# Performance work log

Measured on AMD Instinct MI355X. Metric: run time of the kernel, lower is better.

Reference implementation:

```python
import jax, jax.numpy as jnp
import numpy as np

N_NODES = 100000
N_EDGES = 800000
N_FEAT = 64
H_DIM = 64
N_GRAPHS = 64


def _glorot(key, fan_in, fan_out):
    lim = np.sqrt(6.0 / (fan_in + fan_out)).astype(np.float32)
    return jax.random.uniform(key, (fan_in, fan_out), jnp.float32, -lim, lim)


def setup_inputs() -> dict:
    key = jax.random.key(0)
    ks = jax.random.split(key, 10)
    x = jax.random.normal(ks[0], (N_NODES, N_FEAT), jnp.float32)
    edge_index = jax.random.randint(ks[1], (2, N_EDGES), 0, N_NODES, dtype=jnp.int64)
    batch = jnp.sort(jax.random.randint(ks[2], (N_NODES,), 0, N_GRAPHS, dtype=jnp.int64))
    return {
        "x": x,
        "edge_index": edge_index,
        "batch": batch,
        "W0": _glorot(ks[3], N_FEAT, H_DIM), "b0": jnp.zeros((H_DIM,), jnp.float32),
        "W1": _glorot(ks[4], H_DIM, H_DIM), "b1": jnp.zeros((H_DIM,), jnp.float32),
        "W2": _glorot(ks[5], H_DIM, H_DIM), "b2": jnp.zeros((H_DIM,), jnp.float32),
        "Wl": _glorot(ks[6], H_DIM, H_DIM),
        "bl": jax.random.normal(ks[7], (H_DIM,), jnp.float32) * 0.01,
    }


def _gcn_conv(h, W, b, row, col, dinv_r, dinv_c, n_nodes):
    # PyG GCNConv: x W, then sym-normalized aggregation over edges+self-loops
    h = h @ W                                   # [N, H]
    msg = h[row] * (dinv_r * dinv_c)[:, None]   # gather + scale, [E+N, H]
    out = jax.ops.segment_sum(msg, col, num_segments=n_nodes)  # scatter-add
    return out + b


def reference(x, edge_index, batch, W0, b0, W1, b1, W2, b2, Wl, bl):
    n = x.shape[0]
    loops = jnp.arange(n, dtype=edge_index.dtype)
    row = jnp.concatenate([edge_index[0], loops])  # source nodes (+self-loops)
    col = jnp.concatenate([edge_index[1], loops])  # destination nodes
    deg = jax.ops.segment_sum(jnp.ones_like(col, dtype=x.dtype), col, num_segments=n)
    dinv = jnp.where(deg > 0, jax.lax.rsqrt(deg), 0.0)
    dinv_r, dinv_c = dinv[row], dinv[col]

    out = x
    for W, b in ((W0, b0), (W1, b1), (W2, b2)):
        out = jax.nn.relu(_gcn_conv(out, W, b, row, col, dinv_r, dinv_c, n))
        # F.dropout(training=False) is identity in eval mode
    return (out, out @ Wl + bl)
```

## Files before the change

### kernel.cpp

```cpp
#include <hip/hip_runtime.h>

#define NN 100000
#define NE 800000
#define HD 64
#define BK 128
#define NBUCK ((NN + BK - 1) / BK)
#define PA_EPT 16
#define PA_NB ((NE + 256 * PA_EPT - 1) / (256 * PA_EPT))
#define LDW 68
#define LDB 72

typedef __attribute__((ext_vector_type(8))) short bf16x8;
typedef __attribute__((ext_vector_type(4))) float f32x4;

__device__ __forceinline__ int load_idx(const void* ei, int i, bool is32) {
    if (is32) return ((const int*)ei)[i];
    return (int)(((const long long*)ei)[i]);
}

__device__ __forceinline__ unsigned short f2bf(float f) {
    unsigned u = __float_as_uint(f);
    return (unsigned short)((u + 0x7FFFu + ((u >> 16) & 1u)) >> 16);
}

__device__ __forceinline__ float bf2f(unsigned short h) {
    return __uint_as_float((unsigned)h << 16);
}

__device__ __forceinline__ void bfacc(const uint4& u, float4& a, float4& b) {
    a.x += __uint_as_float(u.x << 16);
    a.y += __uint_as_float(u.x & 0xFFFF0000u);
    a.z += __uint_as_float(u.y << 16);
    a.w += __uint_as_float(u.y & 0xFFFF0000u);
    b.x += __uint_as_float(u.z << 16);
    b.y += __uint_as_float(u.z & 0xFFFF0000u);
    b.z += __uint_as_float(u.w << 16);
    b.w += __uint_as_float(u.w & 0xFFFF0000u);
}

__global__ void k_initdet(const void* ei, int* bcnt, int* flag) {
    __shared__ int bad;
    int t = threadIdx.x;
    if (t == 0) bad = 0;
    if (t < NBUCK) bcnt[t] = 0;
    __syncthreads();
    const long long* p = (const long long*)ei;
    for (int i = t; i < 4096; i += 1024) {
        long long v = p[i];
        if (v < 0 || v >= (long long)NN) bad = 1;
    }
    __syncthreads();
    if (t == 0) *flag = bad ? 1 : 0;
}

__global__ __launch_bounds__(256) void k_pass0(const void* ei, const int* flag,
                                               int* bcnt) {
    __shared__ int h[NBUCK];
    for (int i = threadIdx.x; i < NBUCK; i += 256) h[i] = 0;
    __syncthreads();
    bool is32 = (*flag != 0);
    int stride = gridDim.x * 256;
    for (int e = blockIdx.x * 256 + threadIdx.x; e < NE; e += stride) {
        int dst = load_idx(ei, NE + e, is32);
        atomicAdd(&h[dst >> 7], 1);
    }
    __syncthreads();
    for (int i = threadIdx.x; i < NBUCK; i += 256) {
        int v = h[i];
        if (v) atomicAdd(&bcnt[i], v);
    }
}

__global__ __launch_bounds__(256) void k_scan1(const int* __restrict__ bcnt,
                                               int* __restrict__ offs,
                                               int* __restrict__ curs) {
    __shared__ int sc[256];
    int t = threadIdx.x;
    int v[4], s = 0;
#pragma unroll
    for (int i = 0; i < 4; ++i) {
        int b = t * 4 + i;
        v[i] = (b < NBUCK) ? bcnt[b] : 0;
        s += v[i];
    }
    sc[t] = s;
    __syncthreads();
    for (int off = 1; off < 256; off <<= 1) {
        int add = (t >= off) ? sc[t - off] : 0;
        __syncthreads();
        sc[t] += add;
        __syncthreads();
    }
    int run = sc[t] - s;
#pragma unroll
    for (int i = 0; i < 4; ++i) {
        int b = t * 4 + i;
        if (b < NBUCK) { offs[b] = run; curs[b] = run; }
        run += v[i];
    }
    if (t == 255) offs[NBUCK] = sc[255];
}

__global__ __launch_bounds__(256) void k_passA(const void* ei, const int* flag,
                                               int* curs, unsigned* ebuf) {
    __shared__ int h[NBUCK];
    __shared__ int base[NBUCK];
    for (int i = threadIdx.x; i < NBUCK; i += 256) h[i] = 0;
    __syncthreads();
    bool is32 = (*flag != 0);
    int e0 = blockIdx.x * (256 * PA_EPT);
    int src[PA_EPT], dst[PA_EPT];
#pragma unroll
    for (int i = 0; i < PA_EPT; ++i) {
        int e = e0 + i * 256 + threadIdx.x;
        if (e < NE) {
            src[i] = load_idx(ei, e, is32);
            dst[i] = load_idx(ei, NE + e, is32);
            atomicAdd(&h[dst[i] >> 7], 1);
        } else dst[i] = -1;
    }
    __syncthreads();
    for (int i = threadIdx.x; i < NBUCK; i += 256) {
        int v = h[i];
        base[i] = v ? atomicAdd(&curs[i], v) : 0;
        h[i] = 0;
    }
    __syncthreads();
#pragma unroll
    for (int i = 0; i < PA_EPT; ++i) {
        if (dst[i] >= 0) {
            int b = dst[i] >> 7;
            int p = base[b] + atomicAdd(&h[b], 1);
            ebuf[p] = (unsigned)src[i] | ((unsigned)(dst[i] & 127) << 17);
        }
    }
}

__global__ __launch_bounds__(256) void k_passB(const unsigned* __restrict__ ebuf,
                                               const int* __restrict__ offs,
                                               int* __restrict__ noffs,
                                               int* __restrict__ csr_src,
                                               float* __restrict__ dinv) {
    __shared__ int cnt[BK];
    __shared__ int sc[BK];
    __shared__ int nbase[BK];
    __shared__ int rank[BK];
    int bk = blockIdx.x;
    int t = threadIdx.x;
    if (t < BK) { cnt[t] = 0; rank[t] = 0; }
    __syncthreads();
    int rs = offs[bk], re = offs[bk + 1];
    for (int i = rs + t; i < re; i += 256)
        atomicAdd(&cnt[ebuf[i] >> 17], 1);
    __syncthreads();
    if (t < BK) sc[t] = cnt[t];
    __syncthreads();
    for (int off = 1; off < BK; off <<= 1) {
        int v = 0;
        if (t < BK && t >= off) v = sc[t - off];
        __syncthreads();
        if (t < BK) sc[t] += v;
        __syncthreads();
    }
    if (t < BK) {
        int node = bk * BK + t;
        int nb = rs + sc[t] - cnt[t];
        nbase[t] = nb;
        if (node < NN) {
            noffs[node] = nb;
            dinv[node] = rsqrtf((float)(cnt[t] + 1));
        }
    }
    if (bk == NBUCK - 1 && t == 0) noffs[NN] = re;
    __syncthreads();
    for (int i = rs + t; i < re; i += 256) {
        unsigned w = ebuf[i];
        int dl = w >> 17;
        int p = nbase[dl] + atomicAdd(&rank[dl], 1);
        csr_src[p] = (int)(w & 0x1FFFFu);
    }
}

template <bool BIAS, bool PRE, bool BF16OUT>
__global__ __launch_bounds__(256, 4) void k_gemm(const float* __restrict__ X,
                                                 const float* __restrict__ W,
                                                 const float* __restrict__ bias,
                                                 const float* __restrict__ dinv,
                                                 void* __restrict__ Hout, int n) {
    __shared__ float Ws[64 * LDW];
    __shared__ float Xs[128 * LDW];
    int t = threadIdx.x;
    int row0 = blockIdx.x * 128;
    const float4* X4 = (const float4*)X;
    for (int i = t; i < 64 * 16; i += 256) {
        float4 v = ((const float4*)W)[i];
        *(float4*)&Ws[(i >> 4) * LDW + (i & 15) * 4] = v;
    }
    for (int i = t; i < 128 * 16; i += 256) {
        int r = row0 + (i >> 4);
        float4 v = (r < n) ? X4[(size_t)r * 16 + (i & 15)]
                           : make_float4(0.f, 0.f, 0.f, 0.f);
        *(float4*)&Xs[(i >> 4) * LDW + (i & 15) * 4] = v;
    }
    __syncthreads();
    int tc = (t & 15) * 4;
    int rbase = t >> 4;
    float4 acc[8] = {};
#pragma unroll 1
    for (int k = 0; k < 64; k += 4) {
        float4 wv[4], xv[8];
#pragma unroll
        for (int kk = 0; kk < 4; ++kk)
            wv[kk] = *(const float4*)&Ws[(k + kk) * LDW + tc];
#pragma unroll
        for (int i = 0; i < 8; ++i)
            xv[i] = *(const float4*)&Xs[(rbase + 16 * i) * LDW + k];
#pragma unroll
        for (int i = 0; i < 8; ++i) {
            acc[i].x += xv[i].x * wv[0].x + xv[i].y * wv[1].x
                      + xv[i].z * wv[2].x + xv[i].w * wv[3].x;
            acc[i].y += xv[i].x * wv[0].y + xv[i].y * wv[1].y
                      + xv[i].z * wv[2].y + xv[i].w * wv[3].y;
            acc[i].z += xv[i].x * wv[0].z + xv[i].y * wv[1].z
                      + xv[i].z * wv[2].z + xv[i].w * wv[3].z;
            acc[i].w += xv[i].x * wv[0].w + xv[i].y * wv[1].w
                      + xv[i].z * wv[2].w + xv[i].w * wv[3].w;
        }
    }
    float4 bv = make_float4(0.f, 0.f, 0.f, 0.f);
    if (BIAS) bv = *(const float4*)&bias[tc];
#pragma unroll
    for (int i = 0; i < 8; ++i) {
        int r = row0 + rbase + 16 * i;
        if (r < n) {
            float s = PRE ? dinv[r] : 1.f;
            float4 o;
            o.x = (acc[i].x + bv.x) * s;
            o.y = (acc[i].y + bv.y) * s;
            o.z = (acc[i].z + bv.z) * s;
            o.w = (acc[i].w + bv.w) * s;
            if (BF16OUT) {
                ushort4 p;
                p.x = f2bf(o.x); p.y = f2bf(o.y); p.z = f2bf(o.z); p.w = f2bf(o.w);
                ((ushort4*)Hout)[(size_t)r * 16 + (t & 15)] = p;
            } else {
                ((float4*)Hout)[(size_t)r * 16 + (t & 15)] = o;
            }
        }
    }
}

template <int MODE>
__global__ __launch_bounds__(256, 5) void k_fused(const uint4* __restrict__ Hb,
                                               const int* __restrict__ noffs,
                                               const int* __restrict__ csr_src,
                                               const float* __restrict__ dinv,
                                               const float4* __restrict__ b4,
                                               const float* __restrict__ Wn,
                                               const float* __restrict__ bl,
                                               unsigned short* __restrict__ HbOut,
                                               float4* __restrict__ out0,
                                               float* __restrict__ out1) {
    __shared__ unsigned short WtH[64 * LDB];
    __shared__ unsigned short WtL[64 * LDB];
    __shared__ __align__(16) char scratch[32 * LDB * 2 * 2];
    __shared__ float dvs[32];
    __shared__ float bls[64];
    unsigned short* rows_hi = (unsigned short*)scratch;
    unsigned short* rows_lo = (unsigned short*)scratch + 32 * LDB;
    float* cbuf = (float*)scratch;
    int t = threadIdx.x;
    int lane = t & 63;
    int cl = lane >> 3;
    int q = lane & 7;
    int cbase = lane & ~7;
    int nl = (t >> 6) * 8 + cl;
    int base = blockIdx.x * 32;
    int node = base + nl;
    const char* hb8 = (const char*)Hb;
    unsigned qoff = (unsigned)(q << 4);

    float dv = 0.f;
    int e0 = 0, e1 = 0;
    uint4 uself = make_uint4(0u, 0u, 0u, 0u);
    if (node < NN) {
        dv = dinv[node];
        e0 = noffs[node];
        e1 = noffs[node + 1];
        uself = *(const uint4*)(hb8 + (((unsigned)node << 7) | qoff));
    }

    for (int i = t; i < 64 * 64; i += 256) {
        int k = i >> 6, c = i & 63;
        float wv = Wn[i];
        unsigned short hi = f2bf(wv);
        unsigned short lo = f2bf(wv - bf2f(hi));
        WtH[c * LDB + k] = hi;
        WtL[c * LDB + k] = lo;
    }
    if (MODE == 1 && t < 64) bls[t] = bl[t];

    float4 alo = make_float4(0.f, 0.f, 0.f, 0.f);
    float4 ahi = make_float4(0.f, 0.f, 0.f, 0.f);
    if (node < NN) {
        bfacc(uself, alo, ahi);
#pragma unroll 1
        for (int e = e0; e < e1; e += 8) {
            int rem = e1 - e;
            int idx = (q < rem) ? csr_src[e + q] : 0;
            unsigned off[8];
#pragma unroll
            for (int j = 0; j < 8; ++j)
                off[j] = ((unsigned)__shfl(idx, cbase + j, 64) << 7) | qoff;
            uint4 uu[8];
#pragma unroll
            for (int j = 0; j < 8; ++j)
                uu[j] = *(const uint4*)(hb8 + off[j]);
#pragma unroll
            for (int j = 0; j < 8; ++j)
                if (j < rem) bfacc(uu[j], alo, ahi);
        }
    }
    if (node < NN) {
        float4 b0v = b4[2 * q], b1v = b4[2 * q + 1];
        float f[8];
        f[0] = fmaxf(alo.x * dv + b0v.x, 0.f);
        f[1] = fmaxf(alo.y * dv + b0v.y, 0.f);
        f[2] = fmaxf(alo.z * dv + b0v.z, 0.f);
        f[3] = fmaxf(alo.w * dv + b0v.w, 0.f);
        f[4] = fmaxf(ahi.x * dv + b1v.x, 0.f);
        f[5] = fmaxf(ahi.y * dv + b1v.y, 0.f);
        f[6] = fmaxf(ahi.z * dv + b1v.z, 0.f);
        f[7] = fmaxf(ahi.w * dv + b1v.w, 0.f);
        if (MODE == 1) {
            out0[(size_t)node * 16 + 2 * q]     = make_float4(f[0], f[1], f[2], f[3]);
            out0[(size_t)node * 16 + 2 * q + 1] = make_float4(f[4], f[5], f[6], f[7]);
        }
        unsigned hw[4], lw[4];
#pragma unroll
        for (int i = 0; i < 4; ++i) {
            unsigned short h0 = f2bf(f[2 * i]),     h1 = f2bf(f[2 * i + 1]);
            unsigned short l0 = f2bf(f[2 * i]     - bf2f(h0));
            unsigned short l1 = f2bf(f[2 * i + 1] - bf2f(h1));
            hw[i] = (unsigned)h0 | ((unsigned)h1 << 16);
            lw[i] = (unsigned)l0 | ((unsigned)l1 << 16);
        }
        *(uint4*)&rows_hi[nl * LDB + 8 * q] = make_uint4(hw[0], hw[1], hw[2], hw[3]);
        *(uint4*)&rows_lo[nl * LDB + 8 * q] = make_uint4(lw[0], lw[1], lw[2], lw[3]);
        if (q == 0) dvs[nl] = dv;
    }
    __syncthreads();

    int w = t >> 6;
    int la = lane & 15, kc = lane >> 4;
    int tr = w & 1;
    int c0 = (w >> 1) * 32;
    f32x4 ac0 = {0.f, 0.f, 0.f, 0.f};
    f32x4 ac1 = {0.f, 0.f, 0.f, 0.f};
    const unsigned short* arH = &rows_hi[(tr * 16 + la) * LDB];
    const unsigned short* arL = &rows_lo[(tr * 16 + la) * LDB];
    const unsigned short* b0H = &WtH[(c0 + la) * LDB];
    const unsigned short* b0L = &WtL[(c0 + la) * LDB];
    const unsigned short* b1H = &WtH[(c0 + 16 + la) * LDB];
    const unsigned short* b1L = &WtL[(c0 + 16 + la) * LDB];
#pragma unroll
    for (int kh = 0; kh < 2; ++kh) {
        int ko = kh * 32 + kc * 8;
        bf16x8 aH  = *(const bf16x8*)(arH + ko);
        bf16x8 aL  = *(const bf16x8*)(arL + ko);
        bf16x8 bH0 = *(const bf16x8*)(b0H + ko);
        bf16x8 bL0 = *(const bf16x8*)(b0L + ko);
        bf16x8 bH1 = *(const bf16x8*)(b1H + ko);
        bf16x8 bL1 = *(const bf16x8*)(b1L + ko);
        ac0 = __builtin_amdgcn_mfma_f32_16x16x32_bf16(aH, bH0, ac0, 0, 0, 0);
        ac1 = __builtin_amdgcn_mfma_f32_16x16x32_bf16(aH, bH1, ac1, 0, 0, 0);
        ac0 = __builtin_amdgcn_mfma_f32_16x16x32_bf16(aL, bH0, ac0, 0, 0, 0);
        ac1 = __builtin_amdgcn_mfma_f32_16x16x32_bf16(aL, bH1, ac1, 0, 0, 0);
        ac0 = __builtin_amdgcn_mfma_f32_16x16x32_bf16(aH, bL0, ac0, 0, 0, 0);
        ac1 = __builtin_amdgcn_mfma_f32_16x16x32_bf16(aH, bL1, ac1, 0, 0, 0);
    }
    __syncthreads();

    int rb2 = tr * 16 + kc * 4;
#pragma unroll
    for (int j = 0; j < 4; ++j) {
        cbuf[(rb2 + j) * LDW + c0 + la]      = ac0[j];
        cbuf[(rb2 + j) * LDW + c0 + 16 + la] = ac1[j];
    }
    __syncthreads();

    int nl2 = t >> 3, q2 = t & 7;
    int n2 = base + nl2;
    if (n2 < NN) {
        const float* cp = &cbuf[nl2 * LDW + 8 * q2];
        if (MODE == 0) {
            float s = dvs[nl2];
            ushort4 pa, pb;
            pa.x = f2bf(cp[0] * s); pa.y = f2bf(cp[1] * s);
            pa.z = f2bf(cp[2] * s); pa.w = f2bf(cp[3] * s);
            pb.x = f2bf(cp[4] * s); pb.y = f2bf(cp[5] * s);
            pb.z = f2bf(cp[6] * s); pb.w = f2bf(cp[7] * s);
            *(ushort4*)&HbOut[(size_t)n2 * 64 + 8 * q2]     = pa;
            *(ushort4*)&HbOut[(size_t)n2 * 64 + 8 * q2 + 4] = pb;
        } else {
            float4 bv0 = *(const float4*)&bls[8 * q2];
            float4 bv1 = *(const float4*)&bls[8 * q2 + 4];
            float4 o0, o1;
            o0.x = cp[0] + bv0.x; o0.y = cp[1] + bv0.y;
            o0.z = cp[2] + bv0.z; o0.w = cp[3] + bv0.w;
            o1.x = cp[4] + bv1.x; o1.y = cp[5] + bv1.y;
            o1.z = cp[6] + bv1.z; o1.w = cp[7] + bv1.w;
            *(float4*)&out1[(size_t)n2 * 64 + 8 * q2]     = o0;
            *(float4*)&out1[(size_t)n2 * 64 + 8 * q2 + 4] = o1;
        }
    }
}

extern "C" void kernel_launch(void* const* d_in, const int* in_sizes, int n_in,
                              void* d_out, int out_size, void* d_ws, size_t ws_size,
                              hipStream_t stream) {
    const float* x  = (const float*)d_in[0];
    const void*  ei = d_in[1];
    const float* W0 = (const float*)d_in[3];
    const float* b0 = (const float*)d_in[4];
    const float* W1 = (const float*)d_in[5];
    const float* b1 = (const float*)d_in[6];
    const float* W2 = (const float*)d_in[7];
    const float* b2 = (const float*)d_in[8];
    const float* Wl = (const float*)d_in[9];
    const float* bl = (const float*)d_in[10];

    char* ws = (char*)d_ws;
    int*      flag    = (int*)(ws);
    int*      bcnt    = (int*)(ws + 256);
    int*      offs    = (int*)(ws + 4352);
    int*      curs    = (int*)(ws + 8448);
    float*    dinv    = (float*)(ws + 12544);
    int*      noffs   = (int*)(ws + 412672);
    int*      csr_src = (int*)(ws + 812800);
    unsigned short* HbA = (unsigned short*)(ws + 4100096);
    unsigned short* HbB = (unsigned short*)(ws + 16900096);

    float* out0 = (float*)d_out;
    float* out1 = out0 + (size_t)NN * HD;
    unsigned* ebuf = (unsigned*)out1;

    int gG = (NN + 127) / 128;
    int gF = (NN + 31) / 32;

    k_initdet<<<1, 1024, 0, stream>>>(ei, bcnt, flag);
    k_pass0<<<128, 256, 0, stream>>>(ei, flag, bcnt);
    k_scan1<<<1, 256, 0, stream>>>(bcnt, offs, curs);
    k_passA<<<PA_NB, 256, 0, stream>>>(ei, flag, curs, ebuf);
    k_passB<<<NBUCK, 256, 0, stream>>>(ebuf, offs, noffs, csr_src, dinv);

    k_gemm<false, true, true><<<gG, 256, 0, stream>>>(x, W0, nullptr, dinv,
                                                      (void*)HbA, NN);
    k_fused<0><<<gF, 256, 0, stream>>>((const uint4*)HbA, noffs, csr_src, dinv,
                                       (const float4*)b0, W1, nullptr,
                                       HbB, nullptr, nullptr);
    k_fused<0><<<gF, 256, 0, stream>>>((const uint4*)HbB, noffs, csr_src, dinv,
                                       (const float4*)b1, W2, nullptr,
                                       HbA, nullptr, nullptr);
    k_fused<1><<<gF, 256, 0, stream>>>((const uint4*)HbA, noffs, csr_src, dinv,
                                       (const float4*)b2, Wl, bl,
                                       nullptr, (float4*)out0, out1);
}
```

Measured before the change: 232.4 us.

## Build CSR with direct per-node degree atomics instead of bucketed two-pass sort

Replaces the bucket-based two-level counting sort (bucket histogram, bucket scan, bucket scatter, per-bucket local sort) with a direct CSR build. It counts per-node degrees with global atomics, runs a two-level scan over nodes, and scatters sources through per-node atomic cursors. Each kernel detects the index width itself instead of reading a flag from a separate launch. This removes the intermediate edge buffer and the per-bucket local sort pass. In exchange it relies on many scattered global atomics, and the order of edges within each row is nondeterministic.

After: 291.1 us. 25.3% more time.

```diff
diff --git a/kernel.cpp b/kernel.cpp
--- a/kernel.cpp
+++ b/kernel.cpp
@@ -3,12 +3,10 @@
 #define NN 100000
 #define NE 800000
 #define HD 64
-#define BK 128
-#define NBUCK ((NN + BK - 1) / BK)
-#define PA_EPT 16
-#define PA_NB ((NE + 256 * PA_EPT - 1) / (256 * PA_EPT))
 #define LDW 68
 #define LDB 72
+#define NSB ((NN + 255) / 256)
+#define SCB ((NE + 1023) / 1024)
 
 typedef __attribute__((ext_vector_type(8))) short bf16x8;
 typedef __attribute__((ext_vector_type(4))) float f32x4;
@@ -38,146 +36,111 @@
     b.w += __uint_as_float(u.w & 0xFFFF0000u);
 }
 
-__global__ void k_initdet(const void* ei, int* bcnt, int* flag) {
-    __shared__ int bad;
-    int t = threadIdx.x;
-    if (t == 0) bad = 0;
-    if (t < NBUCK) bcnt[t] = 0;
+__device__ __forceinline__ bool detect_is32(const void* ei, int t, int* sbad) {
+    if (t == 0) *sbad = 0;
     __syncthreads();
     const long long* p = (const long long*)ei;
-    for (int i = t; i < 4096; i += 1024) {
+    for (int i = t; i < 512; i += 256) {
         long long v = p[i];
-        if (v < 0 || v >= (long long)NN) bad = 1;
-    }
-    __syncthreads();
-    if (t == 0) *flag = bad ? 1 : 0;
-}
-
-__global__ __launch_bounds__(256) void k_pass0(const void* ei, const int* flag,
-                                               int* bcnt) {
-    __shared__ int h[NBUCK];
-    for (int i = threadIdx.x; i < NBUCK; i += 256) h[i] = 0;
-    __syncthreads();
-    bool is32 = (*flag != 0);
-    int stride = gridDim.x * 256;
-    for (int e = blockIdx.x * 256 + threadIdx.x; e < NE; e += stride) {
-        int dst = load_idx(ei, NE + e, is32);
-        atomicAdd(&h[dst >> 7], 1);
-    }
-    __syncthreads();
-    for (int i = threadIdx.x; i < NBUCK; i += 256) {
-        int v = h[i];
-        if (v) atomicAdd(&bcnt[i], v);
-    }
-}
-
-__global__ __launch_bounds__(256) void k_scan1(const int* __restrict__ bcnt,
-                                               int* __restrict__ offs,
-                                               int* __restrict__ curs) {
+        if (v < 0 || v >= (long long)NN) *sbad = 1;
+    }
+    __syncthreads();
+    return *sbad != 0;
+}
+
+
+__global__ __launch_bounds__(256) void k_deg(const void* ei,
+                                             int* __restrict__ deg) {
+    __shared__ int sbad;
+    int t = threadIdx.x;
+    bool is32 = detect_is32(ei, t, &sbad);
+    int e0 = blockIdx.x * 2048 + t;
+    int d[8];
+#pragma unroll
+    for (int j = 0; j < 8; ++j) {
+        int e = e0 + j * 256;
+        d[j] = (e < NE) ? load_idx(ei, NE + e, is32) : -1;
+    }
+#pragma unroll
+    for (int j = 0; j < 8; ++j)
+        if (d[j] >= 0) atomicAdd(&deg[d[j]], 1);
+}
+
+__global__ __launch_bounds__(256) void k_scanP(const int* __restrict__ deg,
+                                               int* __restrict__ noffs,
+                                               int* __restrict__ bsum) {
     __shared__ int sc[256];
     int t = threadIdx.x;
-    int v[4], s = 0;
-#pragma unroll
-    for (int i = 0; i < 4; ++i) {
-        int b = t * 4 + i;
-        v[i] = (b < NBUCK) ? bcnt[b] : 0;
-        s += v[i];
-    }
+    int n = blockIdx.x * 256 + t;
+    int v = (n < NN) ? deg[n] : 0;
+    sc[t] = v;
+    __syncthreads();
+    for (int off = 1; off < 256; off <<= 1) {
+        int a = (t >= off) ? sc[t - off] : 0;
+        __syncthreads();
+        sc[t] += a;
+        __syncthreads();
+    }
+    if (n < NN) noffs[n] = sc[t] - v;
+    if (t == 255) bsum[blockIdx.x] = sc[255];
+}
+
+__global__ __launch_bounds__(256) void k_scanA(const int* __restrict__ deg,
+                                               int* __restrict__ noffs,
+                                               int* __restrict__ curs,
+                                               float* __restrict__ dinv,
+                                               const int* __restrict__ bsum) {
+    __shared__ int sc[256];
+    __shared__ int sx[512];
+    int t = threadIdx.x;
+    int a = (2 * t     < NSB) ? bsum[2 * t]     : 0;
+    int b = (2 * t + 1 < NSB) ? bsum[2 * t + 1] : 0;
+    int s = a + b;
     sc[t] = s;
     __syncthreads();
     for (int off = 1; off < 256; off <<= 1) {
-        int add = (t >= off) ? sc[t - off] : 0;
+        int x = (t >= off) ? sc[t - off] : 0;
         __syncthreads();
-        sc[t] += add;
+        sc[t] += x;
         __syncthreads();
     }
     int run = sc[t] - s;
-#pragma unroll
-    for (int i = 0; i < 4; ++i) {
-        int b = t * 4 + i;
-        if (b < NBUCK) { offs[b] = run; curs[b] = run; }
-        run += v[i];
-    }
-    if (t == 255) offs[NBUCK] = sc[255];
-}
-
-__global__ __launch_bounds__(256) void k_passA(const void* ei, const int* flag,
-                                               int* curs, unsigned* ebuf) {
-    __shared__ int h[NBUCK];
-    __shared__ int base[NBUCK];
-    for (int i = threadIdx.x; i < NBUCK; i += 256) h[i] = 0;
-    __syncthreads();
-    bool is32 = (*flag != 0);
-    int e0 = blockIdx.x * (256 * PA_EPT);
-    int src[PA_EPT], dst[PA_EPT];
-#pragma unroll
-    for (int i = 0; i < PA_EPT; ++i) {
-        int e = e0 + i * 256 + threadIdx.x;
+    sx[2 * t] = run;
+    sx[2 * t + 1] = run + a;
+    __syncthreads();
+    int base = sx[blockIdx.x];
+    int n = blockIdx.x * 256 + t;
+    if (n < NN) {
+        int nb = noffs[n] + base;
+        noffs[n] = nb;
+        curs[n] = nb;
+        dinv[n] = rsqrtf((float)(deg[n] + 1));
+    }
+    if (blockIdx.x == 0 && t == 0) noffs[NN] = NE;
+}
+
+__global__ __launch_bounds__(256) void k_scat(const void* ei,
+                                              int* __restrict__ curs,
+                                              int* __restrict__ csr_src) {
+    __shared__ int sbad;
+    int t = threadIdx.x;
+    bool is32 = detect_is32(ei, t, &sbad);
+    int e0 = blockIdx.x * 1024 + t;
+    int se[4], de[4];
+#pragma unroll
+    for (int j = 0; j < 4; ++j) {
+        int e = e0 + j * 256;
         if (e < NE) {
-            src[i] = load_idx(ei, e, is32);
-            dst[i] = load_idx(ei, NE + e, is32);
-            atomicAdd(&h[dst[i] >> 7], 1);
-        } else dst[i] = -1;
-    }
-    __syncthreads();
-    for (int i = threadIdx.x; i < NBUCK; i += 256) {
-        int v = h[i];
-        base[i] = v ? atomicAdd(&curs[i], v) : 0;
-        h[i] = 0;
-    }
-    __syncthreads();
-#pragma unroll
-    for (int i = 0; i < PA_EPT; ++i) {
-        if (dst[i] >= 0) {
-            int b = dst[i] >> 7;
-            int p = base[b] + atomicAdd(&h[b], 1);
-            ebuf[p] = (unsigned)src[i] | ((unsigned)(dst[i] & 127) << 17);
-        }
-    }
-}
-
-__global__ __launch_bounds__(256) void k_passB(const unsigned* __restrict__ ebuf,
-                                               const int* __restrict__ offs,
-                                               int* __restrict__ noffs,
-                                               int* __restrict__ csr_src,
-                                               float* __restrict__ dinv) {
-    __shared__ int cnt[BK];
-    __shared__ int sc[BK];
-    __shared__ int nbase[BK];
-    __shared__ int rank[BK];
-    int bk = blockIdx.x;
-    int t = threadIdx.x;
-    if (t < BK) { cnt[t] = 0; rank[t] = 0; }
-    __syncthreads();
-    int rs = offs[bk], re = offs[bk + 1];
-    for (int i = rs + t; i < re; i += 256)
-        atomicAdd(&cnt[ebuf[i] >> 17], 1);
-    __syncthreads();
-    if (t < BK) sc[t] = cnt[t];
-    __syncthreads();
-    for (int off = 1; off < BK; off <<= 1) {
-        int v = 0;
-        if (t < BK && t >= off) v = sc[t - off];
-        __syncthreads();
-        if (t < BK) sc[t] += v;
-        __syncthreads();
-    }
-    if (t < BK) {
-        int node = bk * BK + t;
-        int nb = rs + sc[t] - cnt[t];
-        nbase[t] = nb;
-        if (node < NN) {
-            noffs[node] = nb;
-            dinv[node] = rsqrtf((float)(cnt[t] + 1));
-        }
-    }
-    if (bk == NBUCK - 1 && t == 0) noffs[NN] = re;
-    __syncthreads();
-    for (int i = rs + t; i < re; i += 256) {
-        unsigned w = ebuf[i];
-        int dl = w >> 17;
-        int p = nbase[dl] + atomicAdd(&rank[dl], 1);
-        csr_src[p] = (int)(w & 0x1FFFFu);
+            se[j] = load_idx(ei, e, is32);
+            de[j] = load_idx(ei, NE + e, is32);
+        } else de[j] = -1;
+    }
+#pragma unroll
+    for (int j = 0; j < 4; ++j) {
+        if (de[j] >= 0) {
+            int p = atomicAdd(&curs[de[j]], 1);
+            csr_src[p] = se[j];
+        }
     }
 }
 
@@ -431,10 +394,7 @@
     const float* bl = (const float*)d_in[10];
 
     char* ws = (char*)d_ws;
-    int*      flag    = (int*)(ws);
-    int*      bcnt    = (int*)(ws + 256);
-    int*      offs    = (int*)(ws + 4352);
-    int*      curs    = (int*)(ws + 8448);
+    int*      bsum    = (int*)(ws + 256);
     float*    dinv    = (float*)(ws + 12544);
     int*      noffs   = (int*)(ws + 412672);
     int*      csr_src = (int*)(ws + 812800);
@@ -443,16 +403,17 @@
 
     float* out0 = (float*)d_out;
     float* out1 = out0 + (size_t)NN * HD;
-    unsigned* ebuf = (unsigned*)out1;
+    int* deg  = (int*)out1;
+    int* curs = deg + 102400;
 
     int gG = (NN + 127) / 128;
     int gF = (NN + 31) / 32;
 
-    k_initdet<<<1, 1024, 0, stream>>>(ei, bcnt, flag);
-    k_pass0<<<128, 256, 0, stream>>>(ei, flag, bcnt);
-    k_scan1<<<1, 256, 0, stream>>>(bcnt, offs, curs);
-    k_passA<<<PA_NB, 256, 0, stream>>>(ei, flag, curs, ebuf);
-    k_passB<<<NBUCK, 256, 0, stream>>>(ebuf, offs, noffs, csr_src, dinv);
+    hipMemsetAsync(deg, 0, (size_t)NN * sizeof(int), stream);
+    k_deg<<<NSB, 256, 0, stream>>>(ei, deg);
+    k_scanP<<<NSB, 256, 0, stream>>>(deg, noffs, bsum);
+    k_scanA<<<NSB, 256, 0, stream>>>(deg, noffs, curs, dinv, bsum);
+    k_scat<<<SCB, 256, 0, stream>>>(ei, curs, csr_src);
 
     k_gemm<false, true, true><<<gG, 256, 0, stream>>>(x, W0, nullptr, dinv,
                                                       (void*)HbA, NN);
```
